# Performance work log

Hardware: AMD Instinct MI355X
Metric: run time of the kernel (lower is better)

Reference implementation:

```python
import jax, jax.numpy as jnp
import numpy as np

N = 100000   # num nodes
E = 1600000  # num edges
D = 128      # input_dim == hidden_dim == output_dim
EPS_BN = 1e-5
EPS_LN = 1e-5


def setup_inputs() -> dict:
    key = jax.random.key(0)
    ks = jax.random.split(key, 20)
    s = 0.05
    x = jax.random.normal(ks[0], (N, D), jnp.float32)
    edge_index = jax.random.randint(ks[1], (2, E), 0, N, dtype=jnp.int64)
    p = lambda k, shape: jax.random.normal(k, shape, jnp.float32) * s
    return {
        "x": x,
        "edge_index": edge_index,
        # GCNConv layers: weight stored [in, out], bias [out]
        "W0": p(ks[2], (D, D)), "b0": jnp.zeros((D,), jnp.float32),
        "W1": p(ks[3], (D, D)), "b1": jnp.zeros((D,), jnp.float32),
        "W2": p(ks[4], (D, D)), "b2": jnp.zeros((D,), jnp.float32),
        # BatchNorm affine params
        "g0": jnp.ones((D,), jnp.float32), "be0": jnp.zeros((D,), jnp.float32),
        "g1": jnp.ones((D,), jnp.float32), "be1": jnp.zeros((D,), jnp.float32),
        # MHA: seq_len=1 -> only v and out projections affect output
        "Wv": p(ks[5], (D, D)), "bv": jnp.zeros((D,), jnp.float32),
        "Wo": p(ks[6], (D, D)), "bo": jnp.zeros((D,), jnp.float32),
        # attention LayerNorm
        "ln_g": jnp.ones((D,), jnp.float32), "ln_b": jnp.zeros((D,), jnp.float32),
    }


def gcn_conv(x, W, b, row, col, n):
    """PyG GCNConv: h = D^-1/2 (A+I) D^-1/2 (x W) + b, symmetric norm with self-loops."""
    h = x @ W  # [N, out]
    deg = jax.ops.segment_sum(jnp.ones((row.shape[0],), h.dtype), col, num_segments=n) + 1.0
    dinv = jax.lax.rsqrt(deg)                                   # [N]
    msg = h[row] * (dinv[row] * dinv[col])[:, None]              # [E, out] gather
    agg = jax.ops.segment_sum(msg, col, num_segments=n)          # [N, out] scatter-add
    return agg + h * (dinv * dinv)[:, None] + b                  # self-loop term + bias


def batch_norm(x, g, b):
    mu = x.mean(0)
    var = x.var(0)
    return (x - mu) * jax.lax.rsqrt(var + EPS_BN) * g + b


def layer_norm(x, g, b):
    mu = x.mean(-1, keepdims=True)
    var = x.var(-1, keepdims=True)
    return (x - mu) * jax.lax.rsqrt(var + EPS_LN) * g + b


def reference(x, edge_index, W0, b0, W1, b1, W2, b2, g0, be0, g1, be1,
              Wv, bv, Wo, bo, ln_g, ln_b):
    row, col = edge_index[0], edge_index[1]
    # layer 0: conv -> BN -> relu -> (+residual; input_dim==hidden so identity residual)
    res = x
    h = gcn_conv(x, W0, b0, row, col, N)
    h = jax.nn.relu(batch_norm(h, g0, be0)) + res
    # middle layer (i=1)
    res = h
    h = gcn_conv(h, W1, b1, row, col, N)
    h = jax.nn.relu(batch_norm(h, g1, be1)) + res
    # MHA over seq_len=1: softmax over a single key is 1, so out = out_proj(v_proj(h))
    att = (h @ Wv + bv) @ Wo + bo
    h = layer_norm(h + att, ln_g, ln_b)
    # output conv
    return gcn_conv(h, W2, b2, row, col, N)
```

## Files before the change

### kernel.cpp

```cpp
#include <hip/hip_runtime.h>
#include <hip/hip_bf16.h>

#define N_NODES 100000
#define N_EDGES 1600000
#define DD 128
#define EPS_BN 1e-5f
#define EPS_LN 1e-5f
#define CAP 48
#define ZROW 100000
#define BIN_BLOCKS 512
#define NTH (BIN_BLOCKS * 256)
#define NBIN 256
#define SUBN 391
#define BCAP2 48
#define BSTRIDE (BIN_BLOCKS * BCAP2)

typedef __attribute__((ext_vector_type(4))) float floatx4;
typedef __attribute__((ext_vector_type(8))) short short8;
typedef __attribute__((ext_vector_type(4))) short short4v;

__device__ inline unsigned short f2bf(float f) {
  unsigned u = __builtin_bit_cast(unsigned, f);
  unsigned r = (u + 0x7FFFu + ((u >> 16) & 1u)) >> 16;
  return (unsigned short)r;
}
__device__ inline float bf2f(unsigned short s) {
  unsigned u = ((unsigned)s) << 16;
  return __builtin_bit_cast(float, u);
}
__device__ inline float bflo(unsigned u) { return __builtin_bit_cast(float, u << 16); }
__device__ inline float bfhi(unsigned u) {
  return __builtin_bit_cast(float, u & 0xFFFF0000u);
}

__global__ __launch_bounds__(1024) void detect_init_kernel(const int* __restrict__ ei,
                                                           int* __restrict__ flag,
                                                           float* __restrict__ sums,
                                                           unsigned* __restrict__ zrow) {
  __shared__ int nz;
  const int tid = threadIdx.x;
  if (tid < 512) sums[tid] = 0.f;
  if (tid < 64) zrow[tid] = 0u;
  if (tid == 0) nz = 0;
  __syncthreads();
  int v = ei[tid * 2 + 1];
  if (v != 0) atomicAdd(&nz, 1);
  __syncthreads();
  if (tid == 0) flag[0] = (nz == 0) ? 1 : 0;
}

__device__ inline void place1(int r, int c, unsigned (*stage)[BCAP2], int* lcnt) {
  unsigned uc = (unsigned)c;
  unsigned bin = uc / SUBN;
  unsigned cl = uc - bin * SUBN;
  int pos = atomicAdd(&lcnt[bin], 1);
  if (pos < BCAP2) stage[bin][pos] = ((unsigned)r << 9) | cl;
}

__global__ __launch_bounds__(256) void bin_stage_kernel(const int* __restrict__ ei,
                                                        const int* __restrict__ flag,
                                                        unsigned* __restrict__ binned,
                                                        int* __restrict__ bcnt) {
  __shared__ unsigned stage[NBIN][BCAP2];
  __shared__ int lcnt[NBIN];
  const int tid = threadIdx.x;
  for (int k = tid; k < NBIN; k += 256) lcnt[k] = 0;
  __syncthreads();

  const int t = blockIdx.x * 256 + tid;
  const int f = flag[0];
  if (f) {
#pragma unroll
    for (int it = 0; it < 7; ++it) {
      int p = t + it * NTH;
      if (p < (N_EDGES / 2)) {
        int4 rv = *(const int4*)(ei + 4 * p);
        int4 cv = *(const int4*)(ei + 2 * N_EDGES + 4 * p);
        place1(rv.x, cv.x, stage, lcnt);
        place1(rv.z, cv.z, stage, lcnt);
      }
    }
  } else {
#pragma unroll
    for (int it = 0; it < 4; ++it) {
      int q = t + it * NTH;
      if (q < (N_EDGES / 4)) {
        int4 rv = *(const int4*)(ei + 4 * q);
        int4 cv = *(const int4*)(ei + N_EDGES + 4 * q);
        place1(rv.x, cv.x, stage, lcnt);
        place1(rv.y, cv.y, stage, lcnt);
        place1(rv.z, cv.z, stage, lcnt);
        place1(rv.w, cv.w, stage, lcnt);
      }
    }
  }
  __syncthreads();

  int n = lcnt[tid] < BCAP2 ? lcnt[tid] : BCAP2;
  unsigned* dst = binned + (size_t)tid * BSTRIDE + blockIdx.x * BCAP2;
  for (int i = 0; i < n; ++i) dst[i] = stage[tid][i];
  bcnt[tid * BIN_BLOCKS + blockIdx.x] = n;
}

__global__ __launch_bounds__(256) void csr_build_kernel(const unsigned* __restrict__ binned,
                                                        const int* __restrict__ bcnt,
                                                        int* __restrict__ cnt,
                                                        unsigned* __restrict__ epos) {
  __shared__ int hist[SUBN];
  __shared__ int lbcnt[BIN_BLOCKS];
  const int tid = threadIdx.x;
  const int bin = blockIdx.x;
  for (int k = tid; k < SUBN; k += 256) hist[k] = 0;
  for (int b = tid; b < BIN_BLOCKS; b += 256) lbcnt[b] = bcnt[bin * BIN_BLOCKS + b];
  __syncthreads();

  const int nbase = bin * SUBN;
  const int nn = (N_NODES - nbase) < SUBN ? (N_NODES - nbase) : SUBN;
  const unsigned* B = binned + (size_t)bin * BSTRIDE;

#pragma unroll
  for (int ii = 0; ii < 6; ++ii) {
    uint4 w[4];
    int idx4[4];
#pragma unroll
    for (int j = 0; j < 4; ++j) {
      idx4[j] = tid + (ii * 4 + j) * 256;
      w[j] = *(const uint4*)(B + idx4[j] * 4);
    }
#pragma unroll
    for (int j = 0; j < 4; ++j) {
      int slice = idx4[j] / 12;
      int slot0 = (idx4[j] - slice * 12) * 4;
      int lim = lbcnt[slice];
      unsigned pw[4] = {w[j].x, w[j].y, w[j].z, w[j].w};
#pragma unroll
      for (int s = 0; s < 4; ++s) {
        if (slot0 + s < lim) {
          unsigned pk = pw[s];
          int cl = (int)(pk & 511u);
          int pos = atomicAdd(&hist[cl], 1);
          if (pos < CAP) epos[(size_t)(nbase + cl) * CAP + pos] = pk >> 9;
        }
      }
    }
  }
  __syncthreads();
  for (int k = tid; k < nn; k += 256) {
    int h = hist[k];
    cnt[nbase + k] = h;
    int d = h < CAP ? h : CAP;
    int dcp = (d + 15) & ~15;
    for (int pos = d; pos < dcp; ++pos)
      epos[(size_t)(nbase + k) * CAP + pos] = ZROW;
  }
}

__global__ void prep_kernel(const float* __restrict__ W0, const float* __restrict__ W1,
                            const float* __restrict__ W2, const float* __restrict__ Wv,
                            const float* __restrict__ Wo, const float* __restrict__ bv,
                            const float* __restrict__ bo, unsigned short* __restrict__ Wt,
                            float* __restrict__ biasp) {
  int id = blockIdx.x * blockDim.x + threadIdx.x;
  if (id < 3 * DD * DD) {
    int mat = id / (DD * DD);
    int rem = id % (DD * DD);
    int k = rem / DD;
    int n = rem % DD;
    const float* W = (mat == 0) ? W0 : (mat == 1) ? W1 : W2;
    Wt[mat * DD * DD + n * DD + k] = f2bf(W[k * DD + n]);
  } else if (id < 4 * DD * DD) {
    int rem = id - 3 * DD * DD;
    int k = rem >> 7, n = rem & 127;
    float acc = 0.f;
    for (int j = 0; j < DD; ++j) acc += Wv[k * DD + j] * Wo[j * DD + n];
    Wt[3 * DD * DD + n * DD + k] = f2bf(acc);
  } else if (id < 4 * DD * DD + DD) {
    int n = id - 4 * DD * DD;
    float acc = bo[n];
    for (int j = 0; j < DD; ++j) acc += bv[j] * Wo[j * DD + n];
    biasp[n] = acc;
  }
}

template <typename AT>
__global__ __launch_bounds__(256) void gemm_bf16_kernel(const AT* __restrict__ A,
                                                        const unsigned short* __restrict__ Wt,
                                                        const int* __restrict__ cnt,
                                                        unsigned short* __restrict__ C) {
  __shared__ short Ws[128][136];
  const int tid = threadIdx.x;
  const int rowbase = blockIdx.x * 128;

#pragma unroll
  for (int i = 0; i < 8; ++i) {
    int ch = tid + i * 256;
    int r = ch >> 4;
    int c = (ch & 15) << 3;
    *(int4*)(&Ws[r][c]) = *(const int4*)(Wt + r * DD + c);
  }

  const int lane = tid & 63;
  const int wv = tid >> 6;
  const int m = lane & 15;
  const int q = lane >> 4;
  const int r0 = wv * 32;

  int row0 = rowbase + r0 + m;
  int row1 = rowbase + r0 + 16 + m;
  if (row0 >= N_NODES) row0 = N_NODES - 1;
  if (row1 >= N_NODES) row1 = N_NODES - 1;
  short8 a0[4], a1[4];
  if constexpr (__is_same(AT, float)) {
    const float* A0 = A + row0 * DD;
    const float* A1 = A + row1 * DD;
#pragma unroll
    for (int kc = 0; kc < 4; ++kc) {
      float4 v0 = *(const float4*)(A0 + kc * 32 + q * 8);
      float4 v1 = *(const float4*)(A0 + kc * 32 + q * 8 + 4);
      float4 w0 = *(const float4*)(A1 + kc * 32 + q * 8);
      float4 w1 = *(const float4*)(A1 + kc * 32 + q * 8 + 4);
      short8 s0, s1;
      s0[0] = (short)f2bf(v0.x); s0[1] = (short)f2bf(v0.y);
      s0[2] = (short)f2bf(v0.z); s0[3] = (short)f2bf(v0.w);
      s0[4] = (short)f2bf(v1.x); s0[5] = (short)f2bf(v1.y);
      s0[6] = (short)f2bf(v1.z); s0[7] = (short)f2bf(v1.w);
      s1[0] = (short)f2bf(w0.x); s1[1] = (short)f2bf(w0.y);
      s1[2] = (short)f2bf(w0.z); s1[3] = (short)f2bf(w0.w);
      s1[4] = (short)f2bf(w1.x); s1[5] = (short)f2bf(w1.y);
      s1[6] = (short)f2bf(w1.z); s1[7] = (short)f2bf(w1.w);
      a0[kc] = s0;
      a1[kc] = s1;
    }
  } else {
    const unsigned short* A0 = A + row0 * DD;
    const unsigned short* A1 = A + row1 * DD;
#pragma unroll
    for (int kc = 0; kc < 4; ++kc) {
      a0[kc] = *(const short8*)(A0 + kc * 32 + q * 8);
      a1[kc] = *(const short8*)(A1 + kc * 32 + q * 8);
    }
  }
  __syncthreads();

  floatx4 acc[2][8];
#pragma unroll
  for (int t = 0; t < 2; ++t)
#pragma unroll
    for (int n = 0; n < 8; ++n) acc[t][n] = (floatx4){0.f, 0.f, 0.f, 0.f};

#pragma unroll
  for (int kc = 0; kc < 4; ++kc) {
    int k = kc * 32 + q * 8;
#pragma unroll
    for (int n = 0; n < 8; ++n) {
      short8 b = *(const short8*)(&Ws[n * 16 + m][k]);
      acc[0][n] = __builtin_amdgcn_mfma_f32_16x16x32_bf16(a0[kc], b, acc[0][n], 0, 0, 0);
      acc[1][n] = __builtin_amdgcn_mfma_f32_16x16x32_bf16(a1[kc], b, acc[1][n], 0, 0, 0);
    }
  }

  __syncthreads();
#pragma unroll
  for (int t = 0; t < 2; ++t) {
#pragma unroll
    for (int r = 0; r < 4; ++r) {
      int rl = r0 + t * 16 + q * 4 + r;
      int row = rowbase + rl;
      float sc = (row < N_NODES) ? rsqrtf((float)cnt[row] + 1.0f) : 0.f;
#pragma unroll
      for (int n = 0; n < 8; ++n) {
        Ws[rl][n * 16 + m] = (short)f2bf(acc[t][n][r] * sc);
      }
    }
  }
  __syncthreads();
#pragma unroll
  for (int i = 0; i < 8; ++i) {
    int ch = tid + i * 256;
    int r = ch >> 4;
    int c = (ch & 15) << 3;
    int row = rowbase + r;
    if (row < N_NODES) *(int4*)(C + row * DD + c) = *(const int4*)(&Ws[r][c]);
  }
}

__global__ __launch_bounds__(256) void gemm_mha_ln_kernel(
    const unsigned short* __restrict__ A, const unsigned short* __restrict__ Wt,
    const float* __restrict__ biasp, const float* __restrict__ lng,
    const float* __restrict__ lnb, unsigned short* __restrict__ C) {
  __shared__ short As[128][136];
  __shared__ short Ws[128][136];
  const int tid = threadIdx.x;
  const int rowbase = blockIdx.x * 128;

#pragma unroll
  for (int i = 0; i < 8; ++i) {
    int ch = tid + i * 256;
    int r = ch >> 4;
    int c = (ch & 15) << 3;
    *(int4*)(&Ws[r][c]) = *(const int4*)(Wt + r * DD + c);
  }
#pragma unroll
  for (int i = 0; i < 8; ++i) {
    int ch = tid + i * 256;
    int r = ch >> 4;
    int c = (ch & 15) << 3;
    int row = rowbase + r;
    int4 v = make_int4(0, 0, 0, 0);
    if (row < N_NODES) v = *(const int4*)(A + row * DD + c);
    *(int4*)(&As[r][c]) = v;
  }
  __syncthreads();

  const int lane = tid & 63;
  const int wv = tid >> 6;
  const int m = lane & 15;
  const int q = lane >> 4;
  const int r0 = wv * 32;

  floatx4 acc[2][8];
#pragma unroll
  for (int t = 0; t < 2; ++t)
#pragma unroll
    for (int n = 0; n < 8; ++n) acc[t][n] = (floatx4){0.f, 0.f, 0.f, 0.f};

#pragma unroll
  for (int kc = 0; kc < 4; ++kc) {
    int k = kc * 32 + q * 8;
    short8 a0 = *(const short8*)(&As[r0 + m][k]);
    short8 a1 = *(const short8*)(&As[r0 + 16 + m][k]);
#pragma unroll
    for (int n = 0; n < 8; ++n) {
      short8 b = *(const short8*)(&Ws[n * 16 + m][k]);
      acc[0][n] = __builtin_amdgcn_mfma_f32_16x16x32_bf16(a0, b, acc[0][n], 0, 0, 0);
      acc[1][n] = __builtin_amdgcn_mfma_f32_16x16x32_bf16(a1, b, acc[1][n], 0, 0, 0);
    }
  }
  __syncthreads();

  float bp[8], gg[8], bb[8];
#pragma unroll
  for (int n = 0; n < 8; ++n) {
    int col = n * 16 + m;
    bp[n] = biasp[col];
    gg[n] = lng[col];
    bb[n] = lnb[col];
  }

#pragma unroll
  for (int t = 0; t < 2; ++t) {
#pragma unroll
    for (int r = 0; r < 4; ++r) {
      int rl = r0 + t * 16 + q * 4 + r;
      float v[8];
      float s = 0.f, ss = 0.f;
#pragma unroll
      for (int n = 0; n < 8; ++n) {
        float val = acc[t][n][r] + bp[n] + bf2f((unsigned short)As[rl][n * 16 + m]);
        v[n] = val;
        s += val;
        ss += val * val;
      }
#pragma unroll
      for (int o = 1; o <= 8; o <<= 1) {
        s += __shfl_xor(s, o, 64);
        ss += __shfl_xor(ss, o, 64);
      }
      float mu = s * (1.f / 128.f);
      float var = ss * (1.f / 128.f) - mu * mu;
      float rs = rsqrtf(var + EPS_LN);
#pragma unroll
      for (int n = 0; n < 8; ++n) {
        Ws[rl][n * 16 + m] = (short)f2bf((v[n] - mu) * rs * gg[n] + bb[n]);
      }
    }
  }
  __syncthreads();
#pragma unroll
  for (int i = 0; i < 8; ++i) {
    int ch = tid + i * 256;
    int r = ch >> 4;
    int c = (ch & 15) << 3;
    int row = rowbase + r;
    if (row < N_NODES) *(int4*)(C + row * DD + c) = *(const int4*)(&Ws[r][c]);
  }
}

template <typename OT>
__global__ __launch_bounds__(256) void aggregate_kernel(const uint4* __restrict__ hw4,
                                                        const unsigned* __restrict__ epos,
                                                        const int* __restrict__ cnt,
                                                        const float* __restrict__ bias,
                                                        OT* __restrict__ out) {
  int node = (blockIdx.x * blockDim.x + threadIdx.x) >> 6;
  int lane = threadIdx.x & 63;
  if (node >= N_NODES) return;
  node = __builtin_amdgcn_readfirstlane(node);
  const int q = lane >> 4;
  const int lc = lane & 15;
  int deg = cnt[node];
  int dc = deg < CAP ? deg : CAP;
  int degc = (dc + 15) & ~15;
  const int s = node * CAP;
  float a[8];
#pragma unroll
  for (int k = 0; k < 8; ++k) a[k] = 0.f;
  for (int p = 0; p < degc; p += 16) {
    int idx[4];
    uint4 u[4];
#pragma unroll
    for (int j = 0; j < 4; ++j) idx[j] = (int)epos[s + p + 4 * j + q];
#pragma unroll
    for (int j = 0; j < 4; ++j) u[j] = hw4[idx[j] * 16 + lc];
#pragma unroll
    for (int j = 0; j < 4; ++j) {
      a[0] += bflo(u[j].x); a[1] += bfhi(u[j].x);
      a[2] += bflo(u[j].y); a[3] += bfhi(u[j].y);
      a[4] += bflo(u[j].z); a[5] += bfhi(u[j].z);
      a[6] += bflo(u[j].w); a[7] += bfhi(u[j].w);
    }
  }
#pragma unroll
  for (int k = 0; k < 8; ++k) {
    a[k] += __shfl_xor(a[k], 16, 64);
    a[k] += __shfl_xor(a[k], 32, 64);
  }
  if (lane < 16) {
    uint4 uh = hw4[node * 16 + lc];
    float dv = rsqrtf((float)deg + 1.0f);
    const float4* b4 = (const float4*)bias;
    float4 bA = b4[2 * lc], bB = b4[2 * lc + 1];
    float o0 = (a[0] + bflo(uh.x)) * dv + bA.x;
    float o1 = (a[1] + bfhi(uh.x)) * dv + bA.y;
    float o2 = (a[2] + bflo(uh.y)) * dv + bA.z;
    float o3 = (a[3] + bfhi(uh.y)) * dv + bA.w;
    float o4 = (a[4] + bflo(uh.z)) * dv + bB.x;
    float o5 = (a[5] + bfhi(uh.z)) * dv + bB.y;
    float o6 = (a[6] + bflo(uh.w)) * dv + bB.z;
    float o7 = (a[7] + bfhi(uh.w)) * dv + bB.w;
    if constexpr (__is_same(OT, float)) {
      float4* o = (float4*)out;
      o[node * 32 + 2 * lc] = make_float4(o0, o1, o2, o3);
      o[node * 32 + 2 * lc + 1] = make_float4(o4, o5, o6, o7);
    } else {
      uint4 w;
      w.x = (unsigned)f2bf(o0) | ((unsigned)f2bf(o1) << 16);
      w.y = (unsigned)f2bf(o2) | ((unsigned)f2bf(o3) << 16);
      w.z = (unsigned)f2bf(o4) | ((unsigned)f2bf(o5) << 16);
      w.w = (unsigned)f2bf(o6) | ((unsigned)f2bf(o7) << 16);
      ((uint4*)out)[node * 16 + lc] = w;
    }
  }
}

__global__ void bn_stats_kernel(const unsigned short* __restrict__ in,
                                float* __restrict__ sum, float* __restrict__ sumsq) {
  int col = threadIdx.x;
  float s = 0.f, ss = 0.f;
  for (int r = blockIdx.x; r < N_NODES; r += gridDim.x) {
    float v = bf2f(in[r * DD + col]);
    s += v;
    ss += v * v;
  }
  atomicAdd(&sum[col], s);
  atomicAdd(&sumsq[col], ss);
}

template <typename RT>
__global__ void bn_norm_kernel(const unsigned short* __restrict__ in,
                               const float* __restrict__ sum, const float* __restrict__ sumsq,
                               const float* __restrict__ g, const float* __restrict__ be,
                               const RT* __restrict__ res, unsigned short* __restrict__ out) {
  int idx = blockIdx.x * blockDim.x + threadIdx.x;
  if (idx >= N_NODES * 32) return;
  int c4 = (idx & 31) << 2;
  short4v v = ((const short4v*)in)[idx];
  float r4[4];
  if constexpr (__is_same(RT, float)) {
    float4 r = ((const float4*)res)[idx];
    r4[0] = r.x; r4[1] = r.y; r4[2] = r.z; r4[3] = r.w;
  } else {
    short4v r = ((const short4v*)res)[idx];
    r4[0] = bf2f((unsigned short)r.x);
    r4[1] = bf2f((unsigned short)r.y);
    r4[2] = bf2f((unsigned short)r.z);
    r4[3] = bf2f((unsigned short)r.w);
  }
  const float invn = 1.0f / (float)N_NODES;
  short4v o;
#pragma unroll
  for (int j = 0; j < 4; ++j) {
    int c = c4 + j;
    float mu = sum[c] * invn;
    float var = sumsq[c] * invn - mu * mu;
    float sc = g[c] * rsqrtf(var + EPS_BN);
    float x = bf2f((unsigned short)((const short*)&v)[j]);
    float y = (x - mu) * sc + be[c];
    y = fmaxf(y, 0.f) + r4[j];
    ((short*)&o)[j] = (short)f2bf(y);
  }
  ((short4v*)out)[idx] = o;
}

extern "C" void kernel_launch(void* const* d_in, const int* in_sizes, int n_in,
                              void* d_out, int out_size, void* d_ws, size_t ws_size,
                              hipStream_t stream) {
  const float* x = (const float*)d_in[0];
  const int* ei = (const int*)d_in[1];
  const float* W0 = (const float*)d_in[2];
  const float* b0 = (const float*)d_in[3];
  const float* W1 = (const float*)d_in[4];
  const float* b1 = (const float*)d_in[5];
  const float* W2 = (const float*)d_in[6];
  const float* b2 = (const float*)d_in[7];
  const float* g0 = (const float*)d_in[8];
  const float* be0 = (const float*)d_in[9];
  const float* g1 = (const float*)d_in[10];
  const float* be1 = (const float*)d_in[11];
  const float* Wv = (const float*)d_in[12];
  const float* bv = (const float*)d_in[13];
  const float* Wo = (const float*)d_in[14];
  const float* bo = (const float*)d_in[15];
  const float* lng = (const float*)d_in[16];
  const float* lnb = (const float*)d_in[17];
  float* outp = (float*)d_out;

  char* w = (char*)d_ws;
  unsigned short* Gb = (unsigned short*)(w + 0);
  unsigned* zrow = (unsigned*)(w + 25600000);
  unsigned short* h1b = (unsigned short*)(w + 25600256);
  unsigned short* h2b = (unsigned short*)(w + 51200256);
  unsigned* epos = (unsigned*)(w + 76800256);
  int* cnt = (int*)(w + 96000256);
  float* sums = (float*)(w + 96400384);
  unsigned short* Wt = (unsigned short*)(w + 96402560);
  float* biasp = (float*)(w + 96533632);
  int* flag = (int*)(w + 96534144);
  unsigned* binned = (unsigned*)Gb;
  int* bcnt = (int*)h1b;
  unsigned short* aggB = (unsigned short*)d_out;

  detect_init_kernel<<<1, 1024, 0, stream>>>(ei, flag, sums, zrow);
  bin_stage_kernel<<<BIN_BLOCKS, 256, 0, stream>>>(ei, flag, binned, bcnt);
  csr_build_kernel<<<NBIN, 256, 0, stream>>>(binned, bcnt, cnt, epos);
  prep_kernel<<<(4 * DD * DD + DD + 255) / 256, 256, 0, stream>>>(W0, W1, W2, Wv, Wo, bv, bo,
                                                                  Wt, biasp);

  const int GB = (N_NODES + 127) / 128;
  const int AB = (N_NODES + 3) / 4;
  const int EB = (N_NODES * 32 + 255) / 256;

  gemm_bf16_kernel<float><<<GB, 256, 0, stream>>>(x, Wt + 0 * DD * DD, cnt, Gb);
  aggregate_kernel<unsigned short><<<AB, 256, 0, stream>>>((const uint4*)Gb, epos, cnt, b0,
                                                           aggB);
  bn_stats_kernel<<<512, 128, 0, stream>>>(aggB, sums + 0, sums + 128);
  bn_norm_kernel<float><<<EB, 256, 0, stream>>>(aggB, sums + 0, sums + 128, g0, be0, x, h1b);

  gemm_bf16_kernel<unsigned short><<<GB, 256, 0, stream>>>(h1b, Wt + 1 * DD * DD, cnt, Gb);
  aggregate_kernel<unsigned short><<<AB, 256, 0, stream>>>((const uint4*)Gb, epos, cnt, b1,
                                                           aggB);
  bn_stats_kernel<<<512, 128, 0, stream>>>(aggB, sums + 256, sums + 384);
  bn_norm_kernel<unsigned short><<<EB, 256, 0, stream>>>(aggB, sums + 256, sums + 384, g1, be1,
                                                         h1b, h2b);

  gemm_mha_ln_kernel<<<GB, 256, 0, stream>>>(h2b, Wt + 3 * DD * DD, biasp, lng, lnb, h1b);

  gemm_bf16_kernel<unsigned short><<<GB, 256, 0, stream>>>(h1b, Wt + 2 * DD * DD, cnt, Gb);
  aggregate_kernel<float><<<AB, 256, 0, stream>>>((const uint4*)Gb, epos, cnt, b2, outp);
}
```

Before: 560.5 us.

## Split GEMM output into 8 column planes and aggregate per plane

The GEMM now writes its bf16 result as 8 column planes of 16 features (32 bytes per row), each with a zero row at the end. The aggregation kernel assigns blocks to one plane, so neighbor gathers touch a compact plane that is more likely to stay in cache. Each wavefront now handles 4 nodes with 16 lanes each, and a grid-stride loop replaces the one-node-per-wave launch. The cost is 8x more index loads and narrower 32-byte gathers, and the binned scratch buffer moves to h2b because Gb grows.

```diff
diff --git a/kernel.cpp b/kernel.cpp
--- a/kernel.cpp
+++ b/kernel.cpp
@@ -8,12 +8,14 @@
 #define EPS_LN 1e-5f
 #define CAP 48
 #define ZROW 100000
+#define NROWS 100001
 #define BIN_BLOCKS 512
 #define NTH (BIN_BLOCKS * 256)
 #define NBIN 256
 #define SUBN 391
 #define BCAP2 48
 #define BSTRIDE (BIN_BLOCKS * BCAP2)
+#define GS_AGG 2048
 
 typedef __attribute__((ext_vector_type(4))) float floatx4;
 typedef __attribute__((ext_vector_type(8))) short short8;
@@ -36,11 +38,14 @@
 __global__ __launch_bounds__(1024) void detect_init_kernel(const int* __restrict__ ei,
                                                            int* __restrict__ flag,
                                                            float* __restrict__ sums,
-                                                           unsigned* __restrict__ zrow) {
+                                                           unsigned* __restrict__ gz) {
   __shared__ int nz;
   const int tid = threadIdx.x;
   if (tid < 512) sums[tid] = 0.f;
-  if (tid < 64) zrow[tid] = 0u;
+  if (tid < 64) {
+    int p = tid >> 3, wd = tid & 7;
+    gz[(size_t)(p * NROWS + ZROW) * 8 + wd] = 0u;
+  }
   if (tid == 0) nz = 0;
   __syncthreads();
   int v = ei[tid * 2 + 1];
@@ -186,7 +191,7 @@
 __global__ __launch_bounds__(256) void gemm_bf16_kernel(const AT* __restrict__ A,
                                                         const unsigned short* __restrict__ Wt,
                                                         const int* __restrict__ cnt,
-                                                        unsigned short* __restrict__ C) {
+                                                        unsigned short* __restrict__ Cp) {
   __shared__ short Ws[128][136];
   const int tid = threadIdx.x;
   const int rowbase = blockIdx.x * 128;
@@ -275,12 +280,16 @@
   }
   __syncthreads();
 #pragma unroll
-  for (int i = 0; i < 8; ++i) {
+  for (int i = 0; i < 4; ++i) {
     int ch = tid + i * 256;
-    int r = ch >> 4;
-    int c = (ch & 15) << 3;
-    int row = rowbase + r;
-    if (row < N_NODES) *(int4*)(C + row * DD + c) = *(const int4*)(&Ws[r][c]);
+    int p = ch >> 7;
+    int rl = ch & 127;
+    int row = rowbase + rl;
+    if (row < N_NODES) {
+      size_t off = ((size_t)(p * NROWS + row)) * 16;
+      *(int4*)(Cp + off) = *(const int4*)(&Ws[rl][p * 16]);
+      *(int4*)(Cp + off + 8) = *(const int4*)(&Ws[rl][p * 16 + 8]);
+    }
   }
 }
 
@@ -387,68 +396,77 @@
 }
 
 template <typename OT>
-__global__ __launch_bounds__(256) void aggregate_kernel(const uint4* __restrict__ hw4,
+__global__ __launch_bounds__(256) void aggregate_kernel(const uint4* __restrict__ gp,
                                                         const unsigned* __restrict__ epos,
                                                         const int* __restrict__ cnt,
                                                         const float* __restrict__ bias,
                                                         OT* __restrict__ out) {
-  int node = (blockIdx.x * blockDim.x + threadIdx.x) >> 6;
-  int lane = threadIdx.x & 63;
-  if (node >= N_NODES) return;
-  node = __builtin_amdgcn_readfirstlane(node);
+  const int plane = blockIdx.x & 7;
+  const int gb = blockIdx.x >> 3;
+  const int tid = threadIdx.x;
+  const int wv = tid >> 6;
+  const int lane = tid & 63;
   const int q = lane >> 4;
-  const int lc = lane & 15;
-  int deg = cnt[node];
-  int dc = deg < CAP ? deg : CAP;
-  int degc = (dc + 15) & ~15;
-  const int s = node * CAP;
-  float a[8];
-#pragma unroll
-  for (int k = 0; k < 8; ++k) a[k] = 0.f;
-  for (int p = 0; p < degc; p += 16) {
-    int idx[4];
-    uint4 u[4];
-#pragma unroll
-    for (int j = 0; j < 4; ++j) idx[j] = (int)epos[s + p + 4 * j + q];
-#pragma unroll
-    for (int j = 0; j < 4; ++j) u[j] = hw4[idx[j] * 16 + lc];
-#pragma unroll
-    for (int j = 0; j < 4; ++j) {
-      a[0] += bflo(u[j].x); a[1] += bfhi(u[j].x);
-      a[2] += bflo(u[j].y); a[3] += bfhi(u[j].y);
-      a[4] += bflo(u[j].z); a[5] += bfhi(u[j].z);
-      a[6] += bflo(u[j].w); a[7] += bfhi(u[j].w);
-    }
-  }
-#pragma unroll
-  for (int k = 0; k < 8; ++k) {
-    a[k] += __shfl_xor(a[k], 16, 64);
-    a[k] += __shfl_xor(a[k], 32, 64);
-  }
-  if (lane < 16) {
-    uint4 uh = hw4[node * 16 + lc];
-    float dv = rsqrtf((float)deg + 1.0f);
-    const float4* b4 = (const float4*)bias;
-    float4 bA = b4[2 * lc], bB = b4[2 * lc + 1];
-    float o0 = (a[0] + bflo(uh.x)) * dv + bA.x;
-    float o1 = (a[1] + bfhi(uh.x)) * dv + bA.y;
-    float o2 = (a[2] + bflo(uh.y)) * dv + bA.z;
-    float o3 = (a[3] + bfhi(uh.y)) * dv + bA.w;
-    float o4 = (a[4] + bflo(uh.z)) * dv + bB.x;
-    float o5 = (a[5] + bfhi(uh.z)) * dv + bB.y;
-    float o6 = (a[6] + bflo(uh.w)) * dv + bB.z;
-    float o7 = (a[7] + bfhi(uh.w)) * dv + bB.w;
-    if constexpr (__is_same(OT, float)) {
-      float4* o = (float4*)out;
-      o[node * 32 + 2 * lc] = make_float4(o0, o1, o2, o3);
-      o[node * 32 + 2 * lc + 1] = make_float4(o4, o5, o6, o7);
-    } else {
-      uint4 w;
-      w.x = (unsigned)f2bf(o0) | ((unsigned)f2bf(o1) << 16);
-      w.y = (unsigned)f2bf(o2) | ((unsigned)f2bf(o3) << 16);
-      w.z = (unsigned)f2bf(o4) | ((unsigned)f2bf(o5) << 16);
-      w.w = (unsigned)f2bf(o6) | ((unsigned)f2bf(o7) << 16);
-      ((uint4*)out)[node * 16 + lc] = w;
+  const int sub = lane & 15;
+  const int slot = sub >> 1;
+  const int h16 = sub & 1;
+  const uint4* P = gp + (size_t)plane * NROWS * 2;
+  const float4* b4 = (const float4*)bias;
+  const float4 bA = b4[plane * 4 + h16 * 2];
+  const float4 bB = b4[plane * 4 + h16 * 2 + 1];
+
+  for (int nb = gb * 16; nb < N_NODES; nb += GS_AGG * 16) {
+    int node = nb + wv * 4 + q;
+    int deg = cnt[node];
+    int dc = deg < CAP ? deg : CAP;
+    int degc = (dc + 15) & ~15;
+    int s = node * CAP;
+    float a[8];
+#pragma unroll
+    for (int k = 0; k < 8; ++k) a[k] = 0.f;
+    for (int p0 = 0; p0 < degc; p0 += 16) {
+      int i0 = (int)epos[s + p0 + slot];
+      int i1 = (int)epos[s + p0 + 8 + slot];
+      uint4 u0 = P[(size_t)i0 * 2 + h16];
+      uint4 u1 = P[(size_t)i1 * 2 + h16];
+      a[0] += bflo(u0.x) + bflo(u1.x);
+      a[1] += bfhi(u0.x) + bfhi(u1.x);
+      a[2] += bflo(u0.y) + bflo(u1.y);
+      a[3] += bfhi(u0.y) + bfhi(u1.y);
+      a[4] += bflo(u0.z) + bflo(u1.z);
+      a[5] += bfhi(u0.z) + bfhi(u1.z);
+      a[6] += bflo(u0.w) + bflo(u1.w);
+      a[7] += bfhi(u0.w) + bfhi(u1.w);
+    }
+#pragma unroll
+    for (int k = 0; k < 8; ++k) {
+      a[k] += __shfl_xor(a[k], 2, 64);
+      a[k] += __shfl_xor(a[k], 4, 64);
+      a[k] += __shfl_xor(a[k], 8, 64);
+    }
+    if (slot == 0) {
+      uint4 uh = P[(size_t)node * 2 + h16];
+      float dv = rsqrtf((float)deg + 1.0f);
+      float o0 = (a[0] + bflo(uh.x)) * dv + bA.x;
+      float o1 = (a[1] + bfhi(uh.x)) * dv + bA.y;
+      float o2 = (a[2] + bflo(uh.y)) * dv + bA.z;
+      float o3 = (a[3] + bfhi(uh.y)) * dv + bA.w;
+      float o4 = (a[4] + bflo(uh.z)) * dv + bB.x;
+      float o5 = (a[5] + bfhi(uh.z)) * dv + bB.y;
+      float o6 = (a[6] + bflo(uh.w)) * dv + bB.z;
+      float o7 = (a[7] + bfhi(uh.w)) * dv + bB.w;
+      if constexpr (__is_same(OT, float)) {
+        float4* o = (float4*)out;
+        o[node * 32 + plane * 4 + h16 * 2] = make_float4(o0, o1, o2, o3);
+        o[node * 32 + plane * 4 + h16 * 2 + 1] = make_float4(o4, o5, o6, o7);
+      } else {
+        uint4 w;
+        w.x = (unsigned)f2bf(o0) | ((unsigned)f2bf(o1) << 16);
+        w.y = (unsigned)f2bf(o2) | ((unsigned)f2bf(o3) << 16);
+        w.z = (unsigned)f2bf(o4) | ((unsigned)f2bf(o5) << 16);
+        w.w = (unsigned)f2bf(o6) | ((unsigned)f2bf(o7) << 16);
+        ((uint4*)out)[node * 16 + plane * 2 + h16] = w;
+      }
     }
   }
 }
@@ -527,7 +545,6 @@
 
   char* w = (char*)d_ws;
   unsigned short* Gb = (unsigned short*)(w + 0);
-  unsigned* zrow = (unsigned*)(w + 25600000);
   unsigned short* h1b = (unsigned short*)(w + 25600256);
   unsigned short* h2b = (unsigned short*)(w + 51200256);
   unsigned* epos = (unsigned*)(w + 76800256);
@@ -536,18 +553,18 @@
   unsigned short* Wt = (unsigned short*)(w + 96402560);
   float* biasp = (float*)(w + 96533632);
   int* flag = (int*)(w + 96534144);
-  unsigned* binned = (unsigned*)Gb;
+  unsigned* binned = (unsigned*)h2b;
   int* bcnt = (int*)h1b;
   unsigned short* aggB = (unsigned short*)d_out;
 
-  detect_init_kernel<<<1, 1024, 0, stream>>>(ei, flag, sums, zrow);
+  detect_init_kernel<<<1, 1024, 0, stream>>>(ei, flag, sums, (unsigned*)Gb);
   bin_stage_kernel<<<BIN_BLOCKS, 256, 0, stream>>>(ei, flag, binned, bcnt);
   csr_build_kernel<<<NBIN, 256, 0, stream>>>(binned, bcnt, cnt, epos);
   prep_kernel<<<(4 * DD * DD + DD + 255) / 256, 256, 0, stream>>>(W0, W1, W2, Wv, Wo, bv, bo,
                                                                   Wt, biasp);
 
   const int GB = (N_NODES + 127) / 128;
-  const int AB = (N_NODES + 3) / 4;
+  const int AB = 8 * GS_AGG;
   const int EB = (N_NODES * 32 + 255) / 256;
 
   gemm_bf16_kernel<float><<<GB, 256, 0, stream>>>(x, Wt + 0 * DD * DD, cnt, Gb);
```

New measurement: 677.6 us. 20.9% more time.

## Process multiple nodes per wavefront in aggregation with software-prefetched edge indices

Applied to the files above, without the earlier changes.

Each wavefront in the aggregate kernel now handles 7 consecutive nodes instead of one. It prefetches the next node's degree and first 16 edge indices while gathering the current node's neighbours, and it also issues the self-row load early. The CSR build now always pads to at least 16 entries, so the first chunk can be loaded unconditionally. This cuts launch and wave-startup overhead and hides index-load latency, at the cost of fewer waves for latency hiding and some serialization within a wave.

```diff
diff --git a/kernel.cpp b/kernel.cpp
--- a/kernel.cpp
+++ b/kernel.cpp
@@ -14,6 +14,8 @@
 #define SUBN 391
 #define BCAP2 48
 #define BSTRIDE (BIN_BLOCKS * BCAP2)
+#define NPW 7
+#define AGG_BLOCKS 3584
 
 typedef __attribute__((ext_vector_type(4))) float floatx4;
 typedef __attribute__((ext_vector_type(8))) short short8;
@@ -150,6 +152,7 @@
     cnt[nbase + k] = h;
     int d = h < CAP ? h : CAP;
     int dcp = (d + 15) & ~15;
+    if (dcp < 16) dcp = 16;
     for (int pos = d; pos < dcp; ++pos)
       epos[(size_t)(nbase + k) * CAP + pos] = ZROW;
   }
@@ -392,26 +395,43 @@
                                                         const int* __restrict__ cnt,
                                                         const float* __restrict__ bias,
                                                         OT* __restrict__ out) {
-  int node = (blockIdx.x * blockDim.x + threadIdx.x) >> 6;
-  int lane = threadIdx.x & 63;
-  if (node >= N_NODES) return;
-  node = __builtin_amdgcn_readfirstlane(node);
+  const int tid = threadIdx.x;
+  const int lane = tid & 63;
   const int q = lane >> 4;
   const int lc = lane & 15;
+  int n0 = (blockIdx.x * 4 + (tid >> 6)) * NPW;
+  if (n0 >= N_NODES) return;
+  n0 = __builtin_amdgcn_readfirstlane(n0);
+  int n1 = n0 + NPW;
+  if (n1 > N_NODES) n1 = N_NODES;
+
+  const float4* b4 = (const float4*)bias;
+  const float4 bA = b4[2 * lc];
+  const float4 bB = b4[2 * lc + 1];
+
+  int node = n0;
   int deg = cnt[node];
-  int dc = deg < CAP ? deg : CAP;
-  int degc = (dc + 15) & ~15;
-  const int s = node * CAP;
-  float a[8];
-#pragma unroll
-  for (int k = 0; k < 8; ++k) a[k] = 0.f;
-  for (int p = 0; p < degc; p += 16) {
-    int idx[4];
+  int idx[4];
+#pragma unroll
+  for (int j = 0; j < 4; ++j) idx[j] = (int)epos[node * CAP + 4 * j + q];
+
+  for (;;) {
+    const int nnode = node + 1;
+    const bool more = nnode < n1;
+    int ndeg = 0;
+    int nidx[4];
+    if (more) {
+      ndeg = cnt[nnode];
+#pragma unroll
+      for (int j = 0; j < 4; ++j) nidx[j] = (int)epos[nnode * CAP + 4 * j + q];
+    }
     uint4 u[4];
 #pragma unroll
-    for (int j = 0; j < 4; ++j) idx[j] = (int)epos[s + p + 4 * j + q];
-#pragma unroll
-    for (int j = 0; j < 4; ++j) u[j] = hw4[idx[j] * 16 + lc];
+    for (int j = 0; j < 4; ++j) u[j] = hw4[(size_t)idx[j] * 16 + lc];
+    uint4 uh = hw4[(size_t)node * 16 + lc];
+    float a[8];
+#pragma unroll
+    for (int k = 0; k < 8; ++k) a[k] = 0.f;
 #pragma unroll
     for (int j = 0; j < 4; ++j) {
       a[0] += bflo(u[j].x); a[1] += bfhi(u[j].x);
@@ -419,37 +439,56 @@
       a[4] += bflo(u[j].z); a[5] += bfhi(u[j].z);
       a[6] += bflo(u[j].w); a[7] += bfhi(u[j].w);
     }
-  }
-#pragma unroll
-  for (int k = 0; k < 8; ++k) {
-    a[k] += __shfl_xor(a[k], 16, 64);
-    a[k] += __shfl_xor(a[k], 32, 64);
-  }
-  if (lane < 16) {
-    uint4 uh = hw4[node * 16 + lc];
-    float dv = rsqrtf((float)deg + 1.0f);
-    const float4* b4 = (const float4*)bias;
-    float4 bA = b4[2 * lc], bB = b4[2 * lc + 1];
-    float o0 = (a[0] + bflo(uh.x)) * dv + bA.x;
-    float o1 = (a[1] + bfhi(uh.x)) * dv + bA.y;
-    float o2 = (a[2] + bflo(uh.y)) * dv + bA.z;
-    float o3 = (a[3] + bfhi(uh.y)) * dv + bA.w;
-    float o4 = (a[4] + bflo(uh.z)) * dv + bB.x;
-    float o5 = (a[5] + bfhi(uh.z)) * dv + bB.y;
-    float o6 = (a[6] + bflo(uh.w)) * dv + bB.z;
-    float o7 = (a[7] + bfhi(uh.w)) * dv + bB.w;
-    if constexpr (__is_same(OT, float)) {
-      float4* o = (float4*)out;
-      o[node * 32 + 2 * lc] = make_float4(o0, o1, o2, o3);
-      o[node * 32 + 2 * lc + 1] = make_float4(o4, o5, o6, o7);
-    } else {
-      uint4 w;
-      w.x = (unsigned)f2bf(o0) | ((unsigned)f2bf(o1) << 16);
-      w.y = (unsigned)f2bf(o2) | ((unsigned)f2bf(o3) << 16);
-      w.z = (unsigned)f2bf(o4) | ((unsigned)f2bf(o5) << 16);
-      w.w = (unsigned)f2bf(o6) | ((unsigned)f2bf(o7) << 16);
-      ((uint4*)out)[node * 16 + lc] = w;
-    }
+    int dc = deg < CAP ? deg : CAP;
+    int degc = (dc + 15) & ~15;
+    for (int p = 16; p < degc; p += 16) {
+      int ix[4];
+      uint4 v[4];
+#pragma unroll
+      for (int j = 0; j < 4; ++j) ix[j] = (int)epos[node * CAP + p + 4 * j + q];
+#pragma unroll
+      for (int j = 0; j < 4; ++j) v[j] = hw4[(size_t)ix[j] * 16 + lc];
+#pragma unroll
+      for (int j = 0; j < 4; ++j) {
+        a[0] += bflo(v[j].x); a[1] += bfhi(v[j].x);
+        a[2] += bflo(v[j].y); a[3] += bfhi(v[j].y);
+        a[4] += bflo(v[j].z); a[5] += bfhi(v[j].z);
+        a[6] += bflo(v[j].w); a[7] += bfhi(v[j].w);
+      }
+    }
+#pragma unroll
+    for (int k = 0; k < 8; ++k) {
+      a[k] += __shfl_xor(a[k], 16, 64);
+      a[k] += __shfl_xor(a[k], 32, 64);
+    }
+    if (lane < 16) {
+      float dv = rsqrtf((float)deg + 1.0f);
+      float o0 = (a[0] + bflo(uh.x)) * dv + bA.x;
+      float o1 = (a[1] + bfhi(uh.x)) * dv + bA.y;
+      float o2 = (a[2] + bflo(uh.y)) * dv + bA.z;
+      float o3 = (a[3] + bfhi(uh.y)) * dv + bA.w;
+      float o4 = (a[4] + bflo(uh.z)) * dv + bB.x;
+      float o5 = (a[5] + bfhi(uh.z)) * dv + bB.y;
+      float o6 = (a[6] + bflo(uh.w)) * dv + bB.z;
+      float o7 = (a[7] + bfhi(uh.w)) * dv + bB.w;
+      if constexpr (__is_same(OT, float)) {
+        float4* o = (float4*)out;
+        o[node * 32 + 2 * lc] = make_float4(o0, o1, o2, o3);
+        o[node * 32 + 2 * lc + 1] = make_float4(o4, o5, o6, o7);
+      } else {
+        uint4 w;
+        w.x = (unsigned)f2bf(o0) | ((unsigned)f2bf(o1) << 16);
+        w.y = (unsigned)f2bf(o2) | ((unsigned)f2bf(o3) << 16);
+        w.z = (unsigned)f2bf(o4) | ((unsigned)f2bf(o5) << 16);
+        w.w = (unsigned)f2bf(o6) | ((unsigned)f2bf(o7) << 16);
+        ((uint4*)out)[node * 16 + lc] = w;
+      }
+    }
+    if (!more) break;
+    node = nnode;
+    deg = ndeg;
+#pragma unroll
+    for (int j = 0; j < 4; ++j) idx[j] = nidx[j];
   }
 }
 
@@ -547,18 +586,17 @@
                                                                   Wt, biasp);
 
   const int GB = (N_NODES + 127) / 128;
-  const int AB = (N_NODES + 3) / 4;
   const int EB = (N_NODES * 32 + 255) / 256;
 
   gemm_bf16_kernel<float><<<GB, 256, 0, stream>>>(x, Wt + 0 * DD * DD, cnt, Gb);
-  aggregate_kernel<unsigned short><<<AB, 256, 0, stream>>>((const uint4*)Gb, epos, cnt, b0,
-                                                           aggB);
+  aggregate_kernel<unsigned short><<<AGG_BLOCKS, 256, 0, stream>>>((const uint4*)Gb, epos, cnt,
+                                                                   b0, aggB);
   bn_stats_kernel<<<512, 128, 0, stream>>>(aggB, sums + 0, sums + 128);
   bn_norm_kernel<float><<<EB, 256, 0, stream>>>(aggB, sums + 0, sums + 128, g0, be0, x, h1b);
 
   gemm_bf16_kernel<unsigned short><<<GB, 256, 0, stream>>>(h1b, Wt + 1 * DD * DD, cnt, Gb);
-  aggregate_kernel<unsigned short><<<AB, 256, 0, stream>>>((const uint4*)Gb, epos, cnt, b1,
-                                                           aggB);
+  aggregate_kernel<unsigned short><<<AGG_BLOCKS, 256, 0, stream>>>((const uint4*)Gb, epos, cnt,
+                                                                   b1, aggB);
   bn_stats_kernel<<<512, 128, 0, stream>>>(aggB, sums + 256, sums + 384);
   bn_norm_kernel<unsigned short><<<EB, 256, 0, stream>>>(aggB, sums + 256, sums + 384, g1, be1,
                                                          h1b, h2b);
@@ -566,5 +604,6 @@
   gemm_mha_ln_kernel<<<GB, 256, 0, stream>>>(h2b, Wt + 3 * DD * DD, biasp, lng, lnb, h1b);
 
   gemm_bf16_kernel<unsigned short><<<GB, 256, 0, stream>>>(h1b, Wt + 2 * DD * DD, cnt, Gb);
-  aggregate_kernel<float><<<AB, 256, 0, stream>>>((const uint4*)Gb, epos, cnt, b2, outp);
-}
+  aggregate_kernel<float><<<AGG_BLOCKS, 256, 0, stream>>>((const uint4*)Gb, epos, cnt, b2,
+                                                          outp);
+}
```

Result: no change. 564.1 us (+0.6%).
